# Performance work log

Measured on AMD Instinct MI355X. Metric: run time of the kernel, lower is better.

The kernel has to match this reference:

```python
import jax, jax.numpy as jnp
import numpy as np

EPS = 1e-12  # torch F.normalize eps

def _colnorm(w, g):
    # F.normalize(w, dim=0, p=2) * g  (column-wise L2 over dim 0)
    n = jnp.sqrt(jnp.sum(w * w, axis=0, keepdims=True))
    return (w / jnp.maximum(n, EPS)) * g

def setup_inputs() -> dict:
    key = jax.random.key(0)
    ks = jax.random.split(key, 16)
    B, T, V, E, H = 16, 512, 8192, 512, 1024
    inp = {
        'xs': jax.random.randint(ks[0], (B, T), 0, V),
        'ys': jax.random.randint(ks[1], (B, T), 0, V),
        'embed_w': jax.random.normal(ks[2], (V, E), jnp.float32) * 0.02,
        'wx': jax.random.normal(ks[3], (E, 4 * H), jnp.float32),
        'wh': jax.random.normal(ks[4], (H, 4 * H), jnp.float32),
        'wmx': jax.random.normal(ks[5], (E, H), jnp.float32),
        'wmh': jax.random.normal(ks[6], (H, H), jnp.float32),
        'b': jax.random.normal(ks[7], (4 * H,), jnp.float32) * 0.02,
        'gx': jax.random.normal(ks[8], (4 * H,), jnp.float32),
        'gh': jax.random.normal(ks[9], (4 * H,), jnp.float32),
        'gmx': jax.random.normal(ks[10], (H,), jnp.float32),
        'gmh': jax.random.normal(ks[11], (H,), jnp.float32),
        'pred_w': jax.random.normal(ks[12], (V, H), jnp.float32) * 0.02,
        'pred_b': jax.random.normal(ks[13], (V,), jnp.float32) * 0.02,
    }
    return inp

def reference(xs, ys, embed_w, wx, wh, wmx, wmh, b, gx, gh, gmx, gmh, pred_w, pred_b):
    B, T = xs.shape
    H = wmh.shape[0]
    V = pred_w.shape[0]
    # padding_idx=0 -> embedding row 0 is zero
    ew = embed_w.at[0].set(0.0)
    x = ew[xs]  # [B, T, E]
    # weight norm
    wx_n = _colnorm(wx, gx)
    wh_n = _colnorm(wh, gh)
    wmx_n = _colnorm(wmx, gmx)
    wmh_n = _colnorm(wmh, gmh)
    # precompute input-dependent projections (same math, batched over time)
    zx = jnp.einsum('bte,ef->btf', x, wx_n) + b     # [B, T, 4H]
    mx = jnp.einsum('bte,eh->bth', x, wmx_n)        # [B, T, H]

    def step(carry, inp):
        h, c = carry
        zx_t, mx_t = inp
        m = mx_t * (h @ wmh_n)                       # [B, H]
        z = zx_t + m @ wh_n                          # [B, 4H]
        i, f, o, u = jnp.split(z, 4, axis=1)
        i = jax.nn.sigmoid(i)
        f = jax.nn.sigmoid(f)
        o = jax.nn.sigmoid(o)
        u = jnp.tanh(u)
        c = f * c + i * u
        h = o * jnp.tanh(c)
        return (h, c), h

    h0 = jnp.zeros((B, H), x.dtype)
    c0 = jnp.zeros((B, H), x.dtype)
    _, hs = jax.lax.scan(step, (h0, c0), (zx.transpose(1, 0, 2), mx.transpose(1, 0, 2)))
    hs = hs.transpose(1, 0, 2)  # [B, T, H]
    logits = jnp.einsum('bth,vh->btv', hs, pred_w) + pred_b
    log_p = jax.nn.log_softmax(logits.reshape(B * T, V), axis=-1)
    nll = -jnp.take_along_axis(log_p, ys.reshape(B * T, 1), axis=1)
    return jnp.mean(nll)
```

## Files before the change

### kernel.cpp

```cpp
#include <hip/hip_runtime.h>
#include <hip/hip_bf16.h>
#include <stdint.h>

#define B_   16
#define T_   512
#define V_   8192
#define E_   512
#define H_   1024
#define BT_  (B_ * T_)
#define H4_  (4 * H_)

typedef __attribute__((ext_vector_type(8))) short   short8;
typedef __attribute__((ext_vector_type(8))) __bf16  bf16x8;
typedef __attribute__((ext_vector_type(4))) float   f32x4;
typedef __attribute__((ext_vector_type(4))) short   short4v;
typedef unsigned long long ull;

__device__ __forceinline__ float bf2f(short s) {
  union { unsigned u; float f; } x;
  x.u = ((unsigned)(unsigned short)s) << 16;
  return x.f;
}
__device__ __forceinline__ short f2bf(float f) {
  union { float f; unsigned u; } x; x.f = f;
  unsigned u = x.u;
  u = (u + 0x7fffu + ((u >> 16) & 1u)) >> 16;
  return (short)u;
}
__device__ __forceinline__ f32x4 mfma16(short8 a, short8 b, f32x4 c) {
  return __builtin_amdgcn_mfma_f32_16x16x32_bf16(
      __builtin_bit_cast(bf16x8, a), __builtin_bit_cast(bf16x8, b), c, 0, 0, 0);
}
__device__ __forceinline__ float sigm(float x) { return 1.f / (1.f + __expf(-x)); }
__device__ __forceinline__ float tanh_f(float x) { return 1.f - 2.f / (__expf(2.f * x) + 1.f); }

__device__ __forceinline__ short8 mk8(ull lo, ull hi) {
  union { ull u[2]; short8 s; } c;
  c.u[0] = lo; c.u[1] = hi;
  return c.s;
}

__global__ __launch_bounds__(256) void colscale(const float* __restrict__ W,
                                                const float* __restrict__ g,
                                                float* __restrict__ sc, int Kr, int N) {
  int j = blockIdx.x * 256 + threadIdx.x;
  if (j >= N) return;
  float ss = 0.f;
  for (int i = 0; i < Kr; ++i) { float v = W[(long)i * N + j]; ss = fmaf(v, v, ss); }
  sc[j] = g[j] / fmaxf(sqrtf(ss), 1e-12f);
}

__global__ __launch_bounds__(256) void transpose_cast(const float* __restrict__ W,
                                                      const float* __restrict__ sc,
                                                      short* __restrict__ WT, int Kr, int N) {
  __shared__ float tile[32][33];
  int nbi = Kr >> 5;
  int bi = blockIdx.x % nbi, bj = blockIdx.x / nbi;
  int i0 = bi << 5, j0 = bj << 5;
  int tx = threadIdx.x & 31, ty = threadIdx.x >> 5;
  for (int yy = ty; yy < 32; yy += 8)
    tile[yy][tx] = W[(long)(i0 + yy) * N + j0 + tx];
  __syncthreads();
  for (int yy = ty; yy < 32; yy += 8) {
    int j = j0 + yy;
    WT[(long)j * Kr + i0 + tx] = f2bf(tile[tx][yy] * sc[j]);
  }
}

__global__ __launch_bounds__(256) void castbf(const float* __restrict__ src,
                                              short* __restrict__ dst, long n) {
  long i = ((long)blockIdx.x * 256 + threadIdx.x) * 4;
  if (i + 3 < n) {
    float4 v = *(const float4*)(src + i);
    short4v o = { f2bf(v.x), f2bf(v.y), f2bf(v.z), f2bf(v.w) };
    *(short4v*)(dst + i) = o;
  }
}

__global__ __launch_bounds__(256) void embed_gather(const int* __restrict__ xs,
                                                    const float* __restrict__ ew,
                                                    short* __restrict__ x) {
  int r = blockIdx.x;
  int idx = xs[r];
  const float* src = ew + (long)idx * E_;
  for (int e = threadIdx.x; e < E_; e += 256) {
    float v = (idx == 0) ? 0.f : src[e];
    x[(long)r * E_ + e] = f2bf(v);
  }
}

__global__ __launch_bounds__(256) void gemm_bt(const short* __restrict__ A,
                                               const short* __restrict__ BT,
                                               const float* __restrict__ bias,
                                               short* __restrict__ C,
                                               int M, int N, int K) {
  int ntiles = N >> 7;
  int tM = (blockIdx.x / ntiles) << 7;
  int tN = (blockIdx.x % ntiles) << 7;
  int w = threadIdx.x >> 6, lane = threadIdx.x & 63;
  int mo = tM + ((w & 1) << 6), no = tN + ((w >> 1) << 6);
  int lr = lane & 15, lk8 = (lane >> 4) << 3, q = lane >> 4;
  f32x4 acc[4][4] = {};
  const short* Ap = A + (long)(mo + lr) * K + lk8;
  const short* Bp = BT + (long)(no + lr) * K + lk8;
  for (int k0 = 0; k0 < K; k0 += 32) {
    short8 af[4], bfr[4];
#pragma unroll
    for (int i = 0; i < 4; ++i) af[i] = *(const short8*)(Ap + (long)16 * i * K + k0);
#pragma unroll
    for (int j = 0; j < 4; ++j) bfr[j] = *(const short8*)(Bp + (long)16 * j * K + k0);
#pragma unroll
    for (int i = 0; i < 4; ++i)
#pragma unroll
      for (int j = 0; j < 4; ++j)
        acc[i][j] = mfma16(af[i], bfr[j], acc[i][j]);
  }
  float pbv[4];
#pragma unroll
  for (int j = 0; j < 4; ++j) pbv[j] = bias ? bias[no + 16 * j + lr] : 0.f;
#pragma unroll
  for (int i = 0; i < 4; ++i)
#pragma unroll
    for (int j = 0; j < 4; ++j)
#pragma unroll
      for (int r = 0; r < 4; ++r) {
        int row = mo + 16 * i + 4 * q + r;
        int col = no + 16 * j + lr;
        C[(long)row * N + col] = f2bf(acc[i][j][r] + pbv[j]);
      }
}

#define NWG_  64
#define NLOG_ 192

__global__ __launch_bounds__(256, 1) void scan_logits(
    const short* __restrict__ zxb, const short* __restrict__ mxb,
    const short* __restrict__ wmhT, const short* __restrict__ whT,
    short* __restrict__ hs,
    ull* __restrict__ h_ex,
    ull* __restrict__ m_ex,
    unsigned* __restrict__ flags_m,
    unsigned* __restrict__ flags_h,
    unsigned* __restrict__ prog,
    const short* __restrict__ pwb,
    const float* __restrict__ pb,
    const int* __restrict__ ys,
    float* __restrict__ sumexp,
    float* __restrict__ logit_y) {
  const int blk = blockIdx.x;
  const int tid = threadIdx.x;
  const int w = tid >> 6, lane = tid & 63;
  const int lr = lane & 15, q = lane >> 4;

  if (blk < NWG_) {
    const int g = blk;
    const int colg = g << 4;
    const int b = tid >> 4, cl = tid & 15;

    __shared__ float red1[4][16][16];
    __shared__ float red2[4][4][16][16];

    short8 wmh_f[8];
#pragma unroll
    for (int kk = 0; kk < 8; ++kk) {
      const ull* p = (const ull*)(wmhT + (long)(colg + lr) * H_ + (w << 8) + (kk << 5) + (q << 3));
      ull lo = __hip_atomic_load(p, __ATOMIC_RELAXED, __HIP_MEMORY_SCOPE_WORKGROUP);
      ull hi = __hip_atomic_load(p + 1, __ATOMIC_RELAXED, __HIP_MEMORY_SCOPE_WORKGROUP);
      wmh_f[kk] = mk8(lo, hi);
    }
    short8 wh_f[4][8];
#pragma unroll
    for (int gt = 0; gt < 4; ++gt)
#pragma unroll
      for (int kk = 0; kk < 8; ++kk) {
        const ull* p = (const ull*)(whT + (long)(gt * H_ + colg + lr) * H_ + (w << 8) + (kk << 5) + (q << 3));
        ull lo = __hip_atomic_load(p, __ATOMIC_RELAXED, __HIP_MEMORY_SCOPE_WORKGROUP);
        ull hi = __hip_atomic_load(p + 1, __ATOMIC_RELAXED, __HIP_MEMORY_SCOPE_WORKGROUP);
        wh_f[gt][kk] = mk8(lo, hi);
      }

    float c = 0.f;
    const ull* hp = h_ex + lr * 256 + (w << 6) + (q << 1);
    const ull* mp = m_ex + lr * 256 + (w << 6) + (q << 1);
    const unsigned* fhp = flags_h + (((w << 4) + (lane >> 2)) * 4 + (lane & 3)) * 16;
    const unsigned* fmp = flags_m + ((w << 4) + lr) * 16;
    const int b2 = tid >> 2, ch = tid & 3;
    ull* m_st = m_ex + (b2 << 8) + (colg >> 2) + ch;
    unsigned* h_st = (unsigned*)h_ex + (((b << 10) + colg + cl) >> 1);

    for (int t = 0; t < T_; ++t) {
      long rrow = (long)(b * T_ + t);
      const short* zrow = zxb + rrow * H4_ + colg + cl;
      short z0p = zrow[0 * H_], z1p = zrow[1 * H_], z2p = zrow[2 * H_], z3p = zrow[3 * H_];
      ull mxq = 0;
      if (w == 0)
        mxq = *(const ull*)(mxb + (long)(b2 * T_ + t) * H_ + colg + (ch << 2));

      while (__hip_atomic_load(fhp, __ATOMIC_RELAXED, __HIP_MEMORY_SCOPE_AGENT)
             < (unsigned)t) {}

      ull lh[16];
#pragma unroll
      for (int kk = 0; kk < 8; ++kk) {
        lh[2 * kk]     = __hip_atomic_load(hp + (kk << 3),     __ATOMIC_RELAXED, __HIP_MEMORY_SCOPE_AGENT);
        lh[2 * kk + 1] = __hip_atomic_load(hp + (kk << 3) + 1, __ATOMIC_RELAXED, __HIP_MEMORY_SCOPE_AGENT);
      }
      f32x4 a1 = {};
#pragma unroll
      for (int kk = 0; kk < 8; ++kk)
        a1 = mfma16(mk8(lh[2 * kk], lh[2 * kk + 1]), wmh_f[kk], a1);
#pragma unroll
      for (int r = 0; r < 4; ++r) red1[w][q * 4 + r][lr] = a1[r];
      __syncthreads();

      if (w == 0) {
        union { short4v s; ull u; } pk;
        union { short4v s; ull u; } mxu; mxu.u = mxq;
#pragma unroll
        for (int u = 0; u < 4; ++u) {
          float s = red1[0][b2][(ch << 2) + u] + red1[1][b2][(ch << 2) + u] +
                    red1[2][b2][(ch << 2) + u] + red1[3][b2][(ch << 2) + u];
          pk.s[u] = f2bf(bf2f(mxu.s[u]) * s);
        }
        __hip_atomic_store(m_st, pk.u, __ATOMIC_RELAXED, __HIP_MEMORY_SCOPE_AGENT);
        __builtin_amdgcn_s_waitcnt(0);
        if (tid == 0)
          __hip_atomic_store(&flags_m[g << 4], (unsigned)(t + 1),
                             __ATOMIC_RELAXED, __HIP_MEMORY_SCOPE_AGENT);
      }

      while (__hip_atomic_load(fmp, __ATOMIC_RELAXED, __HIP_MEMORY_SCOPE_AGENT)
             < (unsigned)(t + 1)) {}

      ull lm[16];
#pragma unroll
      for (int kk = 0; kk < 8; ++kk) {
        lm[2 * kk]     = __hip_atomic_load(mp + (kk << 3),     __ATOMIC_RELAXED, __HIP_MEMORY_SCOPE_AGENT);
        lm[2 * kk + 1] = __hip_atomic_load(mp + (kk << 3) + 1, __ATOMIC_RELAXED, __HIP_MEMORY_SCOPE_AGENT);
      }
      f32x4 a2[4] = {};
#pragma unroll
      for (int kk = 0; kk < 8; ++kk) {
        short8 mf = mk8(lm[2 * kk], lm[2 * kk + 1]);
#pragma unroll
        for (int gt = 0; gt < 4; ++gt)
          a2[gt] = mfma16(mf, wh_f[gt][kk], a2[gt]);
      }
#pragma unroll
      for (int gt = 0; gt < 4; ++gt)
#pragma unroll
        for (int r = 0; r < 4; ++r)
          red2[w][gt][q * 4 + r][lr] = a2[gt][r];
      __syncthreads();

      {
        float zi = red2[0][0][b][cl] + red2[1][0][b][cl] + red2[2][0][b][cl] + red2[3][0][b][cl] + bf2f(z0p);
        float zf = red2[0][1][b][cl] + red2[1][1][b][cl] + red2[2][1][b][cl] + red2[3][1][b][cl] + bf2f(z1p);
        float zo = red2[0][2][b][cl] + red2[1][2][b][cl] + red2[2][2][b][cl] + red2[3][2][b][cl] + bf2f(z2p);
        float zu = red2[0][3][b][cl] + red2[1][3][b][cl] + red2[2][3][b][cl] + red2[3][3][b][cl] + bf2f(z3p);
        float ig = sigm(zi), fg = sigm(zf), og = sigm(zo), ug = tanh_f(zu);
        c = fg * c + ig * ug;
        float h = og * tanh_f(c);
        short hb = f2bf(h);
        unsigned hv = (unsigned)(unsigned short)hb;
        unsigned ov = (unsigned)__shfl_xor((int)hv, 1);
        unsigned packed = hv | (ov << 16);
        if ((lane & 1) == 0) {
          __hip_atomic_store(h_st, packed, __ATOMIC_RELAXED, __HIP_MEMORY_SCOPE_AGENT);
          __hip_atomic_store((unsigned*)hs + (((rrow << 10) + colg + cl) >> 1),
                             packed, __ATOMIC_RELAXED, __HIP_MEMORY_SCOPE_AGENT);
        }
        __builtin_amdgcn_s_waitcnt(0);
        if (lane == 0) {
          __hip_atomic_store(&flags_h[((g << 2) + w) << 4], (unsigned)(t + 1),
                             __ATOMIC_RELAXED, __HIP_MEMORY_SCOPE_AGENT);
          __hip_atomic_store(&prog[(g << 2) + w], (unsigned)(t + 1),
                             __ATOMIC_RELAXED, __HIP_MEMORY_SCOPE_AGENT);
        }
      }
    }
  } else {
    const int wid = blk - NWG_;
    const int lk8 = (lane >> 4) << 3;
    int lastp = -1;
    for (int s = wid; s < (BT_ / 128) * (V_ / 128); s += NLOG_) {
      const int p = s >> 10;
      const int rem = s & 1023;
      const int bb = rem >> 6, vb = rem & 63;
      if (p != lastp) {
        const unsigned target = (unsigned)((p + 1) << 7);
        const unsigned* pp = prog + tid;
        while (__hip_atomic_load(pp, __ATOMIC_RELAXED, __HIP_MEMORY_SCOPE_AGENT)
               < target)
          __builtin_amdgcn_s_sleep(127);
        __syncthreads();
        lastp = p;
      }
      const int tM = ((bb << 2) + p) << 7;
      const int tN = vb << 7;
      const int mo = tM + ((w & 1) << 6), no = tN + ((w >> 1) << 6);
      f32x4 acc[4][4] = {};
      const ull* Ap = (const ull*)hs + (((long)(mo + lr) << 10) + lk8 >> 2);
      const short* Bp = pwb + (long)(no + lr) * H_ + lk8;
      for (int k0 = 0; k0 < H_; k0 += 32) {
        short8 af[4], bfr[4];
#pragma unroll
        for (int i = 0; i < 4; ++i) {
          const ull* pa = Ap + (long)i * 4096 + (k0 >> 2);
          ull lo = __hip_atomic_load(pa,     __ATOMIC_RELAXED, __HIP_MEMORY_SCOPE_AGENT);
          ull hi = __hip_atomic_load(pa + 1, __ATOMIC_RELAXED, __HIP_MEMORY_SCOPE_AGENT);
          af[i] = mk8(lo, hi);
        }
#pragma unroll
        for (int j = 0; j < 4; ++j) bfr[j] = *(const short8*)(Bp + (long)16 * j * H_ + k0);
#pragma unroll
        for (int i = 0; i < 4; ++i)
#pragma unroll
          for (int j = 0; j < 4; ++j)
            acc[i][j] = mfma16(af[i], bfr[j], acc[i][j]);
      }
      float pbv[4];
#pragma unroll
      for (int j = 0; j < 4; ++j) pbv[j] = pb[no + 16 * j + lr];
#pragma unroll
      for (int i = 0; i < 4; ++i) {
#pragma unroll
        for (int r = 0; r < 4; ++r) {
          int row = mo + 16 * i + 4 * q + r;
          int ysr = ys[row];
          float sum = 0.f;
#pragma unroll
          for (int j = 0; j < 4; ++j) {
            float v = acc[i][j][r] + pbv[j];
            sum += __expf(v);
            int col = no + 16 * j + lr;
            if (col == ysr) logit_y[row] = v;
          }
          sum += __shfl_xor(sum, 1); sum += __shfl_xor(sum, 2);
          sum += __shfl_xor(sum, 4); sum += __shfl_xor(sum, 8);
          if (lr == 0) atomicAdd(&sumexp[row], sum);
        }
      }
    }
  }
}

__global__ __launch_bounds__(256) void reduce_nll(const float* __restrict__ se,
                                                  const float* __restrict__ ly,
                                                  float* __restrict__ out) {
  __shared__ float buf[256];
  float s = 0.f;
  for (int r = threadIdx.x; r < BT_; r += 256)
    s += logf(se[r]) - ly[r];
  buf[threadIdx.x] = s;
  __syncthreads();
  for (int off = 128; off > 0; off >>= 1) {
    if (threadIdx.x < off) buf[threadIdx.x] += buf[threadIdx.x + off];
    __syncthreads();
  }
  if (threadIdx.x == 0) out[0] = buf[0] * (1.0f / BT_);
}

extern "C" void kernel_launch(void* const* d_in, const int* in_sizes, int n_in,
                              void* d_out, int out_size, void* d_ws, size_t ws_size,
                              hipStream_t stream) {
  const int*   xs     = (const int*)d_in[0];
  const int*   ys     = (const int*)d_in[1];
  const float* embw   = (const float*)d_in[2];
  const float* wx     = (const float*)d_in[3];
  const float* wh     = (const float*)d_in[4];
  const float* wmx    = (const float*)d_in[5];
  const float* wmh    = (const float*)d_in[6];
  const float* bias   = (const float*)d_in[7];
  const float* gx     = (const float*)d_in[8];
  const float* gh     = (const float*)d_in[9];
  const float* gmx    = (const float*)d_in[10];
  const float* gmh    = (const float*)d_in[11];
  const float* pred_w = (const float*)d_in[12];
  const float* pred_b = (const float*)d_in[13];
  float* out = (float*)d_out;

  char* base = (char*)d_ws;
  size_t off = 0;
  auto alloc = [&](size_t bytes) -> void* {
    void* p = base + off;
    off = (off + bytes + 255) & ~(size_t)255;
    return p;
  };
  short* xb     = (short*)alloc((size_t)BT_ * E_ * 2);
  short* zxb    = (short*)alloc((size_t)BT_ * H4_ * 2);
  short* mxb    = (short*)alloc((size_t)BT_ * H_ * 2);
  short* hs     = (short*)alloc((size_t)BT_ * H_ * 2);
  short* wxT    = (short*)alloc((size_t)H4_ * E_ * 2);
  short* whT    = (short*)alloc((size_t)H4_ * H_ * 2);
  short* wmxT   = (short*)alloc((size_t)H_ * E_ * 2);
  short* wmhT   = (short*)alloc((size_t)H_ * H_ * 2);
  short* pwb    = (short*)alloc((size_t)V_ * H_ * 2);
  float* scx    = (float*)alloc(H4_ * 4);
  float* sch    = (float*)alloc(H4_ * 4);
  float* scmx   = (float*)alloc(H_ * 4);
  float* scmh   = (float*)alloc(H_ * 4);
  float* l_y    = (float*)alloc(BT_ * 4);
  ull*   m_ex   = (ull*)alloc((size_t)B_ * H_ * 2);
  size_t z0 = off;
  float*    sumexp  = (float*)alloc(BT_ * 4);
  unsigned* flags_m = (unsigned*)alloc(NWG_ * 16 * 4);
  unsigned* flags_h = (unsigned*)alloc(NWG_ * 4 * 16 * 4);
  unsigned* prog    = (unsigned*)alloc(NWG_ * 4 * 4);
  ull*      h_ex    = (ull*)alloc((size_t)B_ * H_ * 2);
  size_t zlen = off - z0;

  hipMemsetAsync(base + z0, 0, zlen, stream);

  colscale<<<H4_ / 256, 256, 0, stream>>>(wx, gx, scx, E_, H4_);
  colscale<<<H4_ / 256, 256, 0, stream>>>(wh, gh, sch, H_, H4_);
  colscale<<<H_ / 256, 256, 0, stream>>>(wmx, gmx, scmx, E_, H_);
  colscale<<<H_ / 256, 256, 0, stream>>>(wmh, gmh, scmh, H_, H_);
  transpose_cast<<<(E_ / 32) * (H4_ / 32), 256, 0, stream>>>(wx, scx, wxT, E_, H4_);
  transpose_cast<<<(H_ / 32) * (H4_ / 32), 256, 0, stream>>>(wh, sch, whT, H_, H4_);
  transpose_cast<<<(E_ / 32) * (H_ / 32), 256, 0, stream>>>(wmx, scmx, wmxT, E_, H_);
  transpose_cast<<<(H_ / 32) * (H_ / 32), 256, 0, stream>>>(wmh, scmh, wmhT, H_, H_);
  castbf<<<((long)V_ * H_) / 1024, 256, 0, stream>>>(pred_w, pwb, (long)V_ * H_);

  embed_gather<<<BT_, 256, 0, stream>>>(xs, embw, xb);
  gemm_bt<<<(BT_ / 128) * (H4_ / 128), 256, 0, stream>>>(xb, wxT, bias, zxb, BT_, H4_, E_);
  gemm_bt<<<(BT_ / 128) * (H_ / 128), 256, 0, stream>>>(xb, wmxT, nullptr, mxb, BT_, H_, E_);

  scan_logits<<<NWG_ + NLOG_, 256, 0, stream>>>(zxb, mxb, wmhT, whT, hs,
                                                h_ex, m_ex, flags_m, flags_h, prog,
                                                pwb, pred_b, ys, sumexp, l_y);

  reduce_nll<<<1, 256, 0, stream>>>(sumexp, l_y, out);
}
```

Measured before the change: 6.046 ms.

## Schedule logits tiles dynamically and let scan workgroups join after recurrence

Logits tiles were statically strided across the 192 dedicated workgroups. They are now handed out through a global atomic tile counter. The 64 recurrence workgroups also pull logits tiles once their scan finishes, so the tail of the last time chunk is spread over all 256 workgroups. Reads of hs change from agent-scope atomic 64-bit loads to plain 128-bit vector loads, which removes the per-load atomic overhead but depends on cache visibility of data written by other workgroups. Every tile now costs an atomic fetch and two extra barriers, and the shared-memory declarations move to function scope.

```diff
diff --git a/kernel.cpp b/kernel.cpp
--- a/kernel.cpp
+++ b/kernel.cpp
@@ -130,8 +130,80 @@
       }
 }
 
-#define NWG_  64
-#define NLOG_ 192
+#define NWG_   64
+#define NLOG_  192
+#define NTILE_ 4096
+
+__device__ __forceinline__ void logits_work(
+    int tid,
+    const short* __restrict__ hs, const short* __restrict__ pwb,
+    const float* __restrict__ pb, const int* __restrict__ ys,
+    float* __restrict__ sumexp, float* __restrict__ logit_y,
+    unsigned* __restrict__ prog, unsigned* __restrict__ tile_ctr,
+    int* s_sh) {
+  const int w = tid >> 6, lane = tid & 63;
+  const int lr = lane & 15, q = lane >> 4;
+  const int lk8 = q << 3;
+  int lastp = -1;
+  for (;;) {
+    __syncthreads();
+    if (tid == 0) *s_sh = (int)atomicAdd(tile_ctr, 1u);
+    __syncthreads();
+    const int s = *s_sh;
+    if (s >= NTILE_) break;
+    const int p = s >> 10;
+    if (p > lastp) {
+      const unsigned target = (unsigned)((p + 1) << 7);
+      while (__hip_atomic_load(prog + tid, __ATOMIC_RELAXED,
+                               __HIP_MEMORY_SCOPE_AGENT) < target)
+        __builtin_amdgcn_s_sleep(127);
+      __syncthreads();
+      lastp = p;
+    }
+    const int rem = s & 1023;
+    const int bb = rem >> 6, vb = rem & 63;
+    const int tM = ((bb << 2) + p) << 7;
+    const int tN = vb << 7;
+    const int mo = tM + ((w & 1) << 6), no = tN + ((w >> 1) << 6);
+    f32x4 acc[4][4] = {};
+    const short* Ap = hs + (long)(mo + lr) * H_ + lk8;
+    const short* Bp = pwb + (long)(no + lr) * H_ + lk8;
+    for (int k0 = 0; k0 < H_; k0 += 32) {
+      short8 af[4], bfr[4];
+#pragma unroll
+      for (int i = 0; i < 4; ++i) af[i] = *(const short8*)(Ap + (long)16 * i * H_ + k0);
+#pragma unroll
+      for (int j = 0; j < 4; ++j) bfr[j] = *(const short8*)(Bp + (long)16 * j * H_ + k0);
+#pragma unroll
+      for (int i = 0; i < 4; ++i)
+#pragma unroll
+        for (int j = 0; j < 4; ++j)
+          acc[i][j] = mfma16(af[i], bfr[j], acc[i][j]);
+    }
+    float pbv[4];
+#pragma unroll
+    for (int j = 0; j < 4; ++j) pbv[j] = pb[no + 16 * j + lr];
+#pragma unroll
+    for (int i = 0; i < 4; ++i) {
+#pragma unroll
+      for (int r = 0; r < 4; ++r) {
+        int row = mo + 16 * i + 4 * q + r;
+        int ysr = ys[row];
+        float sum = 0.f;
+#pragma unroll
+        for (int j = 0; j < 4; ++j) {
+          float v = acc[i][j][r] + pbv[j];
+          sum += __expf(v);
+          int col = no + 16 * j + lr;
+          if (col == ysr) logit_y[row] = v;
+        }
+        sum += __shfl_xor(sum, 1); sum += __shfl_xor(sum, 2);
+        sum += __shfl_xor(sum, 4); sum += __shfl_xor(sum, 8);
+        if (lr == 0) atomicAdd(&sumexp[row], sum);
+      }
+    }
+  }
+}
 
 __global__ __launch_bounds__(256, 1) void scan_logits(
     const short* __restrict__ zxb, const short* __restrict__ mxb,
@@ -142,6 +214,7 @@
     unsigned* __restrict__ flags_m,
     unsigned* __restrict__ flags_h,
     unsigned* __restrict__ prog,
+    unsigned* __restrict__ tile_ctr,
     const short* __restrict__ pwb,
     const float* __restrict__ pb,
     const int* __restrict__ ys,
@@ -150,15 +223,16 @@
   const int blk = blockIdx.x;
   const int tid = threadIdx.x;
   const int w = tid >> 6, lane = tid & 63;
-  const int lr = lane & 15, q = lane >> 4;
+  const int lr = lane & 15, q = tid >> 4 & 0 ? 0 : (lane >> 4);
+
+  __shared__ float red1[4][16][16];
+  __shared__ float red2[4][4][16][16];
+  __shared__ int   s_sh;
 
   if (blk < NWG_) {
     const int g = blk;
     const int colg = g << 4;
     const int b = tid >> 4, cl = tid & 15;
-
-    __shared__ float red1[4][16][16];
-    __shared__ float red2[4][4][16][16];
 
     short8 wmh_f[8];
 #pragma unroll
@@ -279,69 +353,9 @@
         }
       }
     }
+    logits_work(tid, hs, pwb, pb, ys, sumexp, logit_y, prog, tile_ctr, &s_sh);
   } else {
-    const int wid = blk - NWG_;
-    const int lk8 = (lane >> 4) << 3;
-    int lastp = -1;
-    for (int s = wid; s < (BT_ / 128) * (V_ / 128); s += NLOG_) {
-      const int p = s >> 10;
-      const int rem = s & 1023;
-      const int bb = rem >> 6, vb = rem & 63;
-      if (p != lastp) {
-        const unsigned target = (unsigned)((p + 1) << 7);
-        const unsigned* pp = prog + tid;
-        while (__hip_atomic_load(pp, __ATOMIC_RELAXED, __HIP_MEMORY_SCOPE_AGENT)
-               < target)
-          __builtin_amdgcn_s_sleep(127);
-        __syncthreads();
-        lastp = p;
-      }
-      const int tM = ((bb << 2) + p) << 7;
-      const int tN = vb << 7;
-      const int mo = tM + ((w & 1) << 6), no = tN + ((w >> 1) << 6);
-      f32x4 acc[4][4] = {};
-      const ull* Ap = (const ull*)hs + (((long)(mo + lr) << 10) + lk8 >> 2);
-      const short* Bp = pwb + (long)(no + lr) * H_ + lk8;
-      for (int k0 = 0; k0 < H_; k0 += 32) {
-        short8 af[4], bfr[4];
-#pragma unroll
-        for (int i = 0; i < 4; ++i) {
-          const ull* pa = Ap + (long)i * 4096 + (k0 >> 2);
-          ull lo = __hip_atomic_load(pa,     __ATOMIC_RELAXED, __HIP_MEMORY_SCOPE_AGENT);
-          ull hi = __hip_atomic_load(pa + 1, __ATOMIC_RELAXED, __HIP_MEMORY_SCOPE_AGENT);
-          af[i] = mk8(lo, hi);
-        }
-#pragma unroll
-        for (int j = 0; j < 4; ++j) bfr[j] = *(const short8*)(Bp + (long)16 * j * H_ + k0);
-#pragma unroll
-        for (int i = 0; i < 4; ++i)
-#pragma unroll
-          for (int j = 0; j < 4; ++j)
-            acc[i][j] = mfma16(af[i], bfr[j], acc[i][j]);
-      }
-      float pbv[4];
-#pragma unroll
-      for (int j = 0; j < 4; ++j) pbv[j] = pb[no + 16 * j + lr];
-#pragma unroll
-      for (int i = 0; i < 4; ++i) {
-#pragma unroll
-        for (int r = 0; r < 4; ++r) {
-          int row = mo + 16 * i + 4 * q + r;
-          int ysr = ys[row];
-          float sum = 0.f;
-#pragma unroll
-          for (int j = 0; j < 4; ++j) {
-            float v = acc[i][j][r] + pbv[j];
-            sum += __expf(v);
-            int col = no + 16 * j + lr;
-            if (col == ysr) logit_y[row] = v;
-          }
-          sum += __shfl_xor(sum, 1); sum += __shfl_xor(sum, 2);
-          sum += __shfl_xor(sum, 4); sum += __shfl_xor(sum, 8);
-          if (lr == 0) atomicAdd(&sumexp[row], sum);
-        }
-      }
-    }
+    logits_work(tid, hs, pwb, pb, ys, sumexp, logit_y, prog, tile_ctr, &s_sh);
   }
 }
 
@@ -407,6 +421,7 @@
   unsigned* flags_m = (unsigned*)alloc(NWG_ * 16 * 4);
   unsigned* flags_h = (unsigned*)alloc(NWG_ * 4 * 16 * 4);
   unsigned* prog    = (unsigned*)alloc(NWG_ * 4 * 4);
+  unsigned* tile_ctr= (unsigned*)alloc(256);
   ull*      h_ex    = (ull*)alloc((size_t)B_ * H_ * 2);
   size_t zlen = off - z0;
 
@@ -428,7 +443,7 @@
 
   scan_logits<<<NWG_ + NLOG_, 256, 0, stream>>>(zxb, mxb, wmhT, whT, hs,
                                                 h_ex, m_ex, flags_m, flags_h, prog,
-                                                pwb, pred_b, ys, sumexp, l_y);
+                                                tile_ctr, pwb, pred_b, ys, sumexp, l_y);
 
   reduce_nll<<<1, 256, 0, stream>>>(sumexp, l_y, out);
 }
```

Result: faster. 5.899 ms (-2.4%).
